# Kernel optimization log

Hardware: AMD Instinct MI355X
Metric: run time of the kernel (lower is better)

## Reference

```python
import jax, jax.numpy as jnp
import numpy as np

B, S, DIM = 8, 4096, 512
G, V = 2, 320            # num_groups, num_vars
CVD = 256                # codevector_dim
D = CVD // G             # per-group codevector dim = 128
TAU = 2.0                # gumbel temperature


def setup_inputs() -> dict:
    key = jax.random.key(0)
    k1, k2, k3, k4 = jax.random.split(key, 4)
    hidden_states = jax.random.normal(k1, (B, S, DIM), dtype=jnp.float32)
    # weight_proj: Linear(dim -> G*V)
    W = jax.random.normal(k2, (DIM, G * V), dtype=jnp.float32) * 0.02
    b = jnp.zeros((G * V,), dtype=jnp.float32)
    # codebook: torch init is uniform(0,1) on [1, G*V, D]; store as [G*V, D]
    codevectors = jax.random.uniform(k3, (G * V, D), dtype=jnp.float32)
    # standard Gumbel(0,1) noise, one row per (token, group)
    u = jax.random.uniform(k4, (B * S * G, V), dtype=jnp.float32,
                           minval=1e-6, maxval=1.0 - 1e-6)
    gumbels = -jnp.log(-jnp.log(u))
    return {"hidden_states": hidden_states, "W": W, "b": b,
            "codevectors": codevectors, "gumbels": gumbels}


def reference(hidden_states, W, b, codevectors, gumbels):
    Bc, Sc, _ = hidden_states.shape
    T = Bc * Sc
    # weight projection -> logits over codebook entries
    logits = hidden_states @ W + b                      # [B, S, G*V]
    flat = logits.reshape(T * G, V)                     # [T*G, V]

    # gumbel_softmax(hard=True) with straight-through estimator
    y_soft = jax.nn.softmax((flat + gumbels) / TAU, axis=-1)
    hard = jax.nn.one_hot(jnp.argmax(y_soft, axis=-1), V, dtype=y_soft.dtype)
    codevector_probs = hard + y_soft - jax.lax.stop_gradient(y_soft)

    # soft distribution (no gumbel noise, no temperature) per torch code
    codevector_dist = jax.nn.softmax(flat.reshape(T, G, V), axis=-1)

    # one-hot weighted sum over codebook = per-group contraction
    cb = codevectors.reshape(G, V, D)                   # [G, V, D]
    out = jnp.einsum('tgv,gvd->tgd',
                     codevector_probs.reshape(T, G, V), cb)
    out = out.reshape(Bc, Sc, G * D)                    # [B, S, codevector_dim]
    return (out, codevector_dist)
```

## Files before the change

kernel.cpp:

```cpp
#include <hip/hip_runtime.h>

#define Tcnt 32768
#define Gn   2
#define Vn   320
#define Dn   128
#define DIMK 512
#define GV   640
#define RB   64

typedef __attribute__((ext_vector_type(8))) short bf16x8;
typedef __attribute__((ext_vector_type(4))) ushort u16x4;
typedef __attribute__((ext_vector_type(4))) float f32x4;

__device__ inline ushort f2bf(float x) {
    unsigned u = __float_as_uint(x);
    return (ushort)((u + 0x7fffu + ((u >> 16) & 1u)) >> 16);
}

#define AS1(p) ((const __attribute__((address_space(1))) void*)(p))
#define AS3(p) ((__attribute__((address_space(3))) void*)(p))

__global__ __launch_bounds__(256) void prep_wt(
    const float* __restrict__ W, ushort* __restrict__ Wt)
{
    __shared__ ushort Ls[64][72];
    int t = blockIdx.x;
    int n0 = (t % 10) * 64, k0 = (t / 10) * 64;
    int ln = threadIdx.x & 63, kq = threadIdx.x >> 6;
    #pragma unroll
    for (int kk = 0; kk < 16; ++kk) {
        int k = kq * 16 + kk;
        Ls[k][ln] = f2bf(W[(size_t)(k0 + k) * GV + n0 + ln]);
    }
    __syncthreads();
    #pragma unroll
    for (int nn = 0; nn < 16; ++nn) {
        int n = kq * 16 + nn;
        Wt[(size_t)(n0 + n) * DIMK + k0 + ln] = Ls[ln][n];
    }
}

__global__ __launch_bounds__(512, 4) void fused_vq_kernel(
    const float*  __restrict__ hs,
    const ushort* __restrict__ Wt,
    const float*  __restrict__ W,
    const float*  __restrict__ bias,
    const float*  __restrict__ gum,
    const float*  __restrict__ cv,
    float* __restrict__ out,
    float* __restrict__ dist)
{
    __shared__ union SMem {
        struct { ushort As[2][RB * 32]; ushort Bs[2][Vn * 32]; } gm;
        float Ls[32][324];
    } U;
    __shared__ int    s_cnt[RB];
    __shared__ int    s_col[RB][8];
    __shared__ float  s_gm[RB][8];
    __shared__ int    s_bidx[RB];

    const int tid = threadIdx.x, w = tid >> 6, lane = tid & 63;
    const int Q = lane >> 4, c16 = lane & 15;
    const int wm = (w >> 1) * 16, wn = (w & 1) * 160;

    const int bid = blockIdx.x;
    const int swz = (bid & 7) * 128 + (bid >> 3);
    const int g = swz & 1;
    const size_t t0 = (size_t)(swz >> 1) * RB;

    if (tid < RB) s_cnt[tid] = 0;

    const int arow_s = tid >> 3, pc = tid & 7;
    const int lq = (pc >> 1) ^ ((arow_s >> 1) & 3);
    const int lc = lq * 2 + (pc & 1);
    const float* asrc = hs + (t0 + arow_s) * DIMK + lc * 4;
    const ushort* wtg = Wt + (size_t)g * Vn * DIMK;

    auto stageB = [&](int buf, int k0) {
        #pragma unroll
        for (int i2 = 0; i2 < 2; ++i2) {
            int s = i2 * 512 + tid;
            int n = s >> 2, pq = s & 3, lqq = pq ^ ((n >> 1) & 3);
            __builtin_amdgcn_global_load_lds(
                AS1(wtg + (size_t)n * DIMK + k0 + lqq * 8),
                AS3(&U.gm.Bs[buf][s * 8]), 16, 0, 0);
        }
        if (w < 4) {
            int s = 1024 + tid;
            int n = s >> 2, pq = s & 3, lqq = pq ^ ((n >> 1) & 3);
            __builtin_amdgcn_global_load_lds(
                AS1(wtg + (size_t)n * DIMK + k0 + lqq * 8),
                AS3(&U.gm.Bs[buf][s * 8]), 16, 0, 0);
        }
    };
    auto writeA = [&](int buf, float4 v) {
        u16x4 o;
        o[0] = f2bf(v.x); o[1] = f2bf(v.y); o[2] = f2bf(v.z); o[3] = f2bf(v.w);
        *(u16x4*)&U.gm.As[buf][tid * 4] = o;
    };

    float4 areg0 = *(const float4*)(asrc);
    stageB(0, 0);
    float4 areg1 = *(const float4*)(asrc + 32);
    writeA(0, areg0);
    __syncthreads();

    f32x4 acc[10];
    #pragma unroll
    for (int j = 0; j < 10; ++j) acc[j] = (f32x4){0.f, 0.f, 0.f, 0.f};

    #pragma unroll
    for (int ks = 0; ks < 16; ++ks) {
        if (ks + 2 < 16) {
            if ((ks & 1) == 0) areg0 = *(const float4*)(asrc + (ks + 2) * 32);
            else               areg1 = *(const float4*)(asrc + (ks + 2) * 32);
        }
        if (ks + 1 < 16) stageB((ks + 1) & 1, (ks + 1) * 32);

        const ushort* Ab = U.gm.As[ks & 1];
        const ushort* Bb = U.gm.Bs[ks & 1];
        const int ar = wm + c16;
        bf16x8 af = *(const bf16x8*)&Ab[(ar * 4 + (Q ^ ((ar >> 1) & 3))) * 8];
        #pragma unroll
        for (int j = 0; j < 10; ++j) {
            int n = wn + j * 16 + c16;
            bf16x8 bv = *(const bf16x8*)&Bb[(n * 4 + (Q ^ ((n >> 1) & 3))) * 8];
            acc[j] = __builtin_amdgcn_mfma_f32_16x16x32_bf16(af, bv, acc[j], 0, 0, 0);
        }
        if (ks + 1 < 16) writeA((ks + 1) & 1, ((ks + 1) & 1) ? areg1 : areg0);
        __syncthreads();
    }

    #pragma unroll
    for (int j = 0; j < 10; ++j) {
        float bb = bias[g * Vn + wn + j * 16 + c16];
        acc[j][0] += bb; acc[j][1] += bb; acc[j][2] += bb; acc[j][3] += bb;
    }

    const float MARGIN = 0.0625f;

    #pragma unroll
    for (int grp = 0; grp < 2; ++grp) {
        __syncthreads();
        if ((w >> 2) == grp) {
            #pragma unroll
            for (int qr = 0; qr < 4; ++qr) {
                int lrow = (wm - grp * 32) + Q * 4 + qr;
                #pragma unroll
                for (int j = 0; j < 10; ++j)
                    U.Ls[lrow][wn + j * 16 + c16] = acc[j][qr];
            }
        }
        __syncthreads();
        for (int ri = 0; ri < 4; ++ri) {
            int rl = w * 4 + ri;
            int row = grp * 32 + rl;
            size_t r2 = (t0 + row) * 2 + g;
            const float* gr = gum + r2 * Vn;
            float lg[5], sv[5];
            #pragma unroll
            for (int j = 0; j < 5; ++j) {
                lg[j] = U.Ls[rl][lane + j * 64];
                sv[j] = lg[j] + gr[lane + j * 64];
            }
            float mxl = -1e30f, mxs = -1e30f; int bi = 0;
            #pragma unroll
            for (int j = 0; j < 5; ++j) {
                mxl = fmaxf(mxl, lg[j]);
                if (sv[j] > mxs) { mxs = sv[j]; bi = lane + j * 64; }
            }
            #pragma unroll
            for (int off = 1; off < 64; off <<= 1) {
                mxl = fmaxf(mxl, __shfl_xor(mxl, off));
                float os = __shfl_xor(mxs, off); int ob = __shfl_xor(bi, off);
                if (os > mxs || (os == mxs && ob < bi)) { mxs = os; bi = ob; }
            }
            float ev[5]; float sum = 0.f;
            #pragma unroll
            for (int j = 0; j < 5; ++j) { ev[j] = __expf(lg[j] - mxl); sum += ev[j]; }
            #pragma unroll
            for (int off = 1; off < 64; off <<= 1) sum += __shfl_xor(sum, off);
            float inv = 1.0f / sum;
            float* dr = dist + r2 * Vn;
            #pragma unroll
            for (int j = 0; j < 5; ++j) dr[lane + j * 64] = ev[j] * inv;

            if (lane == 0) s_bidx[row] = bi;
            float thr = mxs - MARGIN;
            int tot = 0;
            #pragma unroll
            for (int j = 0; j < 5; ++j)
                tot += __popcll(__ballot(sv[j] >= thr));
            if (tot > 1) {
                #pragma unroll
                for (int j = 0; j < 5; ++j) {
                    if (sv[j] >= thr) {
                        int pos = atomicAdd(&s_cnt[row], 1);
                        if (pos < 8) {
                            s_col[row][pos] = lane + j * 64;
                            s_gm[row][pos]  = sv[j] - lg[j];
                        }
                    }
                }
            }
        }
    }
    __syncthreads();

    for (int ui = 0; ui < 8; ++ui) {
        int u = w * 8 + ui;
        int c = s_cnt[u];
        if (c > 1) {
            if (c > 8) c = 8;
            size_t t = t0 + u;
            const float* hr = hs + t * DIMK;
            float4 h0 = *(const float4*)(hr + lane * 8);
            float4 h1 = *(const float4*)(hr + lane * 8 + 4);
            float hv[8] = {h0.x, h0.y, h0.z, h0.w, h1.x, h1.y, h1.z, h1.w};
            float best = -1e30f; int bv2 = 1 << 30;
            for (int j = 0; j < c; ++j) {
                int v = s_col[u][j];
                int gcol = g * Vn + v;
                const float* wc = W + gcol;
                float p = 0.f;
                #pragma unroll
                for (int i = 0; i < 8; ++i)
                    p = fmaf(hv[i], wc[(size_t)(lane * 8 + i) * GV], p);
                #pragma unroll
                for (int off = 1; off < 64; off <<= 1) p += __shfl_xor(p, off);
                float se = p + bias[gcol] + s_gm[u][j];
                if (se > best || (se == best && v < bv2)) { best = se; bv2 = v; }
            }
            if (lane == 0) s_bidx[u] = bv2;
        }
    }
    __syncthreads();

    for (int ui = 0; ui < 8; ++ui) {
        int u = w * 8 + ui;
        size_t t = t0 + u;
        int b = s_bidx[u];
        const float2* cvr = (const float2*)(cv + ((size_t)(g * Vn + b)) * Dn);
        float2 val = cvr[lane];
        *(float2*)(out + t * (Gn * Dn) + g * Dn + lane * 2) = val;
    }
}

extern "C" void kernel_launch(void* const* d_in, const int* in_sizes, int n_in,
                              void* d_out, int out_size, void* d_ws, size_t ws_size,
                              hipStream_t stream) {
    const float* hs  = (const float*)d_in[0];
    const float* W   = (const float*)d_in[1];
    const float* b   = (const float*)d_in[2];
    const float* cv  = (const float*)d_in[3];
    const float* gum = (const float*)d_in[4];

    float* out  = (float*)d_out;
    float* dist = out + (size_t)Tcnt * (Gn * Dn);
    ushort* Wt  = (ushort*)d_ws;

    prep_wt<<<80, 256, 0, stream>>>(W, Wt);
    fused_vq_kernel<<<(Tcnt / RB) * Gn, 512, 0, stream>>>(hs, Wt, W, b, gum, cv, out, dist);
}
```

Measured before the change: 113.2 us.

## Load A fragments directly to registers and inline tie-break refinement per row

```diff
diff --git a/kernel.cpp b/kernel.cpp
--- a/kernel.cpp
+++ b/kernel.cpp
@@ -1,4 +1,5 @@
 #include <hip/hip_runtime.h>
+#include <hip/hip_bf16.h>
 
 #define Tcnt 32768
 #define Gn   2
@@ -9,12 +10,22 @@
 #define RB   64
 
 typedef __attribute__((ext_vector_type(8))) short bf16x8;
-typedef __attribute__((ext_vector_type(4))) ushort u16x4;
+typedef __attribute__((ext_vector_type(8))) ushort u16x8;
 typedef __attribute__((ext_vector_type(4))) float f32x4;
 
 __device__ inline ushort f2bf(float x) {
     unsigned u = __float_as_uint(x);
     return (ushort)((u + 0x7fffu + ((u >> 16) & 1u)) >> 16);
+}
+__device__ inline ushort nbf(float x) {
+    __hip_bfloat16 h = __float2bfloat16(x);
+    return *reinterpret_cast<ushort*>(&h);
+}
+__device__ inline bf16x8 cvt8(float4 a, float4 b) {
+    u16x8 o;
+    o[0]=nbf(a.x); o[1]=nbf(a.y); o[2]=nbf(a.z); o[3]=nbf(a.w);
+    o[4]=nbf(b.x); o[5]=nbf(b.y); o[6]=nbf(b.z); o[7]=nbf(b.w);
+    return (bf16x8)o;
 }
 
 #define AS1(p) ((const __attribute__((address_space(1))) void*)(p))
@@ -50,14 +61,10 @@
     float* __restrict__ out,
     float* __restrict__ dist)
 {
-    __shared__ union SMem {
-        struct { ushort As[2][RB * 32]; ushort Bs[2][Vn * 32]; } gm;
-        float Ls[32][324];
+    __shared__ union {
+        ushort Bs[2][Vn * 32];
+        float  Ls2[320][33];
     } U;
-    __shared__ int    s_cnt[RB];
-    __shared__ int    s_col[RB][8];
-    __shared__ float  s_gm[RB][8];
-    __shared__ int    s_bidx[RB];
 
     const int tid = threadIdx.x, w = tid >> 6, lane = tid & 63;
     const int Q = lane >> 4, c16 = lane & 15;
@@ -68,42 +75,34 @@
     const int g = swz & 1;
     const size_t t0 = (size_t)(swz >> 1) * RB;
 
-    if (tid < RB) s_cnt[tid] = 0;
-
-    const int arow_s = tid >> 3, pc = tid & 7;
-    const int lq = (pc >> 1) ^ ((arow_s >> 1) & 3);
-    const int lc = lq * 2 + (pc & 1);
-    const float* asrc = hs + (t0 + arow_s) * DIMK + lc * 4;
     const ushort* wtg = Wt + (size_t)g * Vn * DIMK;
-
-    auto stageB = [&](int buf, int k0) {
-        #pragma unroll
-        for (int i2 = 0; i2 < 2; ++i2) {
-            int s = i2 * 512 + tid;
-            int n = s >> 2, pq = s & 3, lqq = pq ^ ((n >> 1) & 3);
-            __builtin_amdgcn_global_load_lds(
-                AS1(wtg + (size_t)n * DIMK + k0 + lqq * 8),
-                AS3(&U.gm.Bs[buf][s * 8]), 16, 0, 0);
-        }
-        if (w < 4) {
-            int s = 1024 + tid;
-            int n = s >> 2, pq = s & 3, lqq = pq ^ ((n >> 1) & 3);
-            __builtin_amdgcn_global_load_lds(
-                AS1(wtg + (size_t)n * DIMK + k0 + lqq * 8),
-                AS3(&U.gm.Bs[buf][s * 8]), 16, 0, 0);
+    const float*  abase = hs + (t0 + wm + c16) * DIMK + Q * 8;
+
+    auto stage = [&](int buf, int k0) {
+        {
+            int s = tid;
+            int n = s >> 2, pq = s & 3, lq = pq ^ ((n >> 1) & 3);
+            __builtin_amdgcn_global_load_lds(AS1(wtg + (size_t)n * DIMK + k0 + lq * 8),
+                                             AS3(&U.Bs[buf][s * 8]), 16, 0, 0);
+        }
+        {
+            int s = tid + 512;
+            int n = s >> 2, pq = s & 3, lq = pq ^ ((n >> 1) & 3);
+            __builtin_amdgcn_global_load_lds(AS1(wtg + (size_t)n * DIMK + k0 + lq * 8),
+                                             AS3(&U.Bs[buf][s * 8]), 16, 0, 0);
+        }
+        if (tid < 256) {
+            int s = tid + 1024;
+            int n = s >> 2, pq = s & 3, lq = pq ^ ((n >> 1) & 3);
+            __builtin_amdgcn_global_load_lds(AS1(wtg + (size_t)n * DIMK + k0 + lq * 8),
+                                             AS3(&U.Bs[buf][s * 8]), 16, 0, 0);
         }
     };
-    auto writeA = [&](int buf, float4 v) {
-        u16x4 o;
-        o[0] = f2bf(v.x); o[1] = f2bf(v.y); o[2] = f2bf(v.z); o[3] = f2bf(v.w);
-        *(u16x4*)&U.gm.As[buf][tid * 4] = o;
-    };
-
-    float4 areg0 = *(const float4*)(asrc);
-    stageB(0, 0);
-    float4 areg1 = *(const float4*)(asrc + 32);
-    writeA(0, areg0);
-    __syncthreads();
+
+    stage(0, 0);
+    float4 aC0 = *(const float4*)(abase);
+    float4 aC1 = *(const float4*)(abase + 4);
+    float4 aN0, aN1;
 
     f32x4 acc[10];
     #pragma unroll
@@ -111,24 +110,30 @@
 
     #pragma unroll
     for (int ks = 0; ks < 16; ++ks) {
-        if (ks + 2 < 16) {
-            if ((ks & 1) == 0) areg0 = *(const float4*)(asrc + (ks + 2) * 32);
-            else               areg1 = *(const float4*)(asrc + (ks + 2) * 32);
-        }
-        if (ks + 1 < 16) stageB((ks + 1) & 1, (ks + 1) * 32);
-
-        const ushort* Ab = U.gm.As[ks & 1];
-        const ushort* Bb = U.gm.Bs[ks & 1];
-        const int ar = wm + c16;
-        bf16x8 af = *(const bf16x8*)&Ab[(ar * 4 + (Q ^ ((ar >> 1) & 3))) * 8];
+        if (ks < 15) {
+            stage((ks + 1) & 1, (ks + 1) * 32);
+            aN0 = *(const float4*)(abase + (ks + 1) * 32);
+            aN1 = *(const float4*)(abase + (ks + 1) * 32 + 4);
+        }
+        if (ks < 15) {
+            if (w < 4) asm volatile("s_waitcnt vmcnt(5)" ::: "memory");
+            else       asm volatile("s_waitcnt vmcnt(4)" ::: "memory");
+        } else {
+            asm volatile("s_waitcnt vmcnt(0)" ::: "memory");
+        }
+        __builtin_amdgcn_s_barrier();
+        __builtin_amdgcn_sched_barrier(0);
+
+        bf16x8 af = cvt8(aC0, aC1);
+        const ushort* Bb = U.Bs[ks & 1];
         #pragma unroll
         for (int j = 0; j < 10; ++j) {
             int n = wn + j * 16 + c16;
             bf16x8 bv = *(const bf16x8*)&Bb[(n * 4 + (Q ^ ((n >> 1) & 3))) * 8];
             acc[j] = __builtin_amdgcn_mfma_f32_16x16x32_bf16(af, bv, acc[j], 0, 0, 0);
         }
-        if (ks + 1 < 16) writeA((ks + 1) & 1, ((ks + 1) & 1) ? areg1 : areg0);
-        __syncthreads();
+        __builtin_amdgcn_s_barrier();
+        aC0 = aN0; aC1 = aN1;
     }
 
     #pragma unroll
@@ -137,30 +142,36 @@
         acc[j][0] += bb; acc[j][1] += bb; acc[j][2] += bb; acc[j][3] += bb;
     }
 
+    __syncthreads();
+
     const float MARGIN = 0.0625f;
 
     #pragma unroll
     for (int grp = 0; grp < 2; ++grp) {
+        if ((w >> 2) == grp) {
+            int lrow = wm - grp * 32 + Q * 4;
+            #pragma unroll
+            for (int j = 0; j < 10; ++j) {
+                int col = wn + j * 16 + c16;
+                U.Ls2[col][lrow + 0] = acc[j][0];
+                U.Ls2[col][lrow + 1] = acc[j][1];
+                U.Ls2[col][lrow + 2] = acc[j][2];
+                U.Ls2[col][lrow + 3] = acc[j][3];
+            }
+        }
         __syncthreads();
-        if ((w >> 2) == grp) {
-            #pragma unroll
-            for (int qr = 0; qr < 4; ++qr) {
-                int lrow = (wm - grp * 32) + Q * 4 + qr;
-                #pragma unroll
-                for (int j = 0; j < 10; ++j)
-                    U.Ls[lrow][wn + j * 16 + c16] = acc[j][qr];
-            }
-        }
-        __syncthreads();
+
+        #pragma unroll
         for (int ri = 0; ri < 4; ++ri) {
-            int rl = w * 4 + ri;
-            int row = grp * 32 + rl;
-            size_t r2 = (t0 + row) * 2 + g;
+            int r = w * 4 + ri;
+            size_t trow = t0 + grp * 32 + r;
+            size_t r2 = trow * 2 + g;
             const float* gr = gum + r2 * Vn;
+
             float lg[5], sv[5];
             #pragma unroll
             for (int j = 0; j < 5; ++j) {
-                lg[j] = U.Ls[rl][lane + j * 64];
+                lg[j] = U.Ls2[lane + j * 64][r];
                 sv[j] = lg[j] + gr[lane + j * 64];
             }
             float mxl = -1e30f, mxs = -1e30f; int bi = 0;
@@ -185,64 +196,44 @@
             #pragma unroll
             for (int j = 0; j < 5; ++j) dr[lane + j * 64] = ev[j] * inv;
 
-            if (lane == 0) s_bidx[row] = bi;
             float thr = mxs - MARGIN;
-            int tot = 0;
-            #pragma unroll
-            for (int j = 0; j < 5; ++j)
-                tot += __popcll(__ballot(sv[j] >= thr));
-            if (tot > 1) {
+            unsigned long long mj[5];
+            int cnt = 0;
+            #pragma unroll
+            for (int j = 0; j < 5; ++j) { mj[j] = __ballot(sv[j] >= thr); cnt += __popcll(mj[j]); }
+            if (cnt > 1) {
+                const float* hr = hs + trow * DIMK;
+                float4 h0 = *(const float4*)(hr + lane * 8);
+                float4 h1 = *(const float4*)(hr + lane * 8 + 4);
+                float hv[8] = {h0.x, h0.y, h0.z, h0.w, h1.x, h1.y, h1.z, h1.w};
+                float best = -1e30f; int bv2 = 1 << 30;
                 #pragma unroll
                 for (int j = 0; j < 5; ++j) {
-                    if (sv[j] >= thr) {
-                        int pos = atomicAdd(&s_cnt[row], 1);
-                        if (pos < 8) {
-                            s_col[row][pos] = lane + j * 64;
-                            s_gm[row][pos]  = sv[j] - lg[j];
-                        }
+                    unsigned long long m = mj[j];
+                    while (m) {
+                        int ln = __ffsll((long long)m) - 1; m &= m - 1;
+                        int v = ln + j * 64;
+                        float gmv = __shfl(sv[j] - lg[j], ln);
+                        int gcol = g * Vn + v;
+                        const float* wc = W + gcol;
+                        float p = 0.f;
+                        #pragma unroll
+                        for (int i = 0; i < 8; ++i)
+                            p = fmaf(hv[i], wc[(size_t)(lane * 8 + i) * GV], p);
+                        #pragma unroll
+                        for (int off = 1; off < 64; off <<= 1) p += __shfl_xor(p, off);
+                        float se = p + bias[gcol] + gmv;
+                        if (se > best || (se == best && v < bv2)) { best = se; bv2 = v; }
                     }
                 }
-            }
-        }
-    }
-    __syncthreads();
-
-    for (int ui = 0; ui < 8; ++ui) {
-        int u = w * 8 + ui;
-        int c = s_cnt[u];
-        if (c > 1) {
-            if (c > 8) c = 8;
-            size_t t = t0 + u;
-            const float* hr = hs + t * DIMK;
-            float4 h0 = *(const float4*)(hr + lane * 8);
-            float4 h1 = *(const float4*)(hr + lane * 8 + 4);
-            float hv[8] = {h0.x, h0.y, h0.z, h0.w, h1.x, h1.y, h1.z, h1.w};
-            float best = -1e30f; int bv2 = 1 << 30;
-            for (int j = 0; j < c; ++j) {
-                int v = s_col[u][j];
-                int gcol = g * Vn + v;
-                const float* wc = W + gcol;
-                float p = 0.f;
-                #pragma unroll
-                for (int i = 0; i < 8; ++i)
-                    p = fmaf(hv[i], wc[(size_t)(lane * 8 + i) * GV], p);
-                #pragma unroll
-                for (int off = 1; off < 64; off <<= 1) p += __shfl_xor(p, off);
-                float se = p + bias[gcol] + s_gm[u][j];
-                if (se > best || (se == best && v < bv2)) { best = se; bv2 = v; }
-            }
-            if (lane == 0) s_bidx[u] = bv2;
-        }
-    }
-    __syncthreads();
-
-    for (int ui = 0; ui < 8; ++ui) {
-        int u = w * 8 + ui;
-        size_t t = t0 + u;
-        int b = s_bidx[u];
-        const float2* cvr = (const float2*)(cv + ((size_t)(g * Vn + b)) * Dn);
-        float2 val = cvr[lane];
-        *(float2*)(out + t * (Gn * Dn) + g * Dn + lane * 2) = val;
+                bi = bv2;
+            }
+
+            const float2* cvr = (const float2*)(cv + ((size_t)(g * Vn + bi)) * Dn);
+            float2 val = cvr[lane];
+            *(float2*)(out + trow * (Gn * Dn) + g * Dn + lane * 2) = val;
+        }
+        __syncthreads();
     }
 }
 
```

Measured after the change: 114.6 us. About the same (+1.3%).

## Double row tile to 128 with 1024-thread blocks and inline near-tie refinement

Applied to the files above, without the earlier changes.

```diff
diff --git a/kernel.cpp b/kernel.cpp
--- a/kernel.cpp
+++ b/kernel.cpp
@@ -6,7 +6,7 @@
 #define Dn   128
 #define DIMK 512
 #define GV   640
-#define RB   64
+#define RB   128
 
 typedef __attribute__((ext_vector_type(8))) short bf16x8;
 typedef __attribute__((ext_vector_type(4))) ushort u16x4;
@@ -40,7 +40,7 @@
     }
 }
 
-__global__ __launch_bounds__(512, 4) void fused_vq_kernel(
+__global__ __launch_bounds__(1024, 4) void fused_vq_kernel(
     const float*  __restrict__ hs,
     const ushort* __restrict__ Wt,
     const float*  __restrict__ W,
@@ -50,25 +50,20 @@
     float* __restrict__ out,
     float* __restrict__ dist)
 {
-    __shared__ union SMem {
+    union SMem {
         struct { ushort As[2][RB * 32]; ushort Bs[2][Vn * 32]; } gm;
-        float Ls[32][324];
-    } U;
-    __shared__ int    s_cnt[RB];
-    __shared__ int    s_col[RB][8];
-    __shared__ float  s_gm[RB][8];
-    __shared__ int    s_bidx[RB];
+        float Ls2[Vn][33];
+    };
+    __shared__ SMem U;
 
     const int tid = threadIdx.x, w = tid >> 6, lane = tid & 63;
     const int Q = lane >> 4, c16 = lane & 15;
     const int wm = (w >> 1) * 16, wn = (w & 1) * 160;
 
     const int bid = blockIdx.x;
-    const int swz = (bid & 7) * 128 + (bid >> 3);
+    const int swz = (bid & 7) * 64 + (bid >> 3);
     const int g = swz & 1;
     const size_t t0 = (size_t)(swz >> 1) * RB;
-
-    if (tid < RB) s_cnt[tid] = 0;
 
     const int arow_s = tid >> 3, pc = tid & 7;
     const int lq = (pc >> 1) ^ ((arow_s >> 1) & 3);
@@ -77,15 +72,14 @@
     const ushort* wtg = Wt + (size_t)g * Vn * DIMK;
 
     auto stageB = [&](int buf, int k0) {
-        #pragma unroll
-        for (int i2 = 0; i2 < 2; ++i2) {
-            int s = i2 * 512 + tid;
+        {
+            int s = tid;
             int n = s >> 2, pq = s & 3, lqq = pq ^ ((n >> 1) & 3);
             __builtin_amdgcn_global_load_lds(
                 AS1(wtg + (size_t)n * DIMK + k0 + lqq * 8),
                 AS3(&U.gm.Bs[buf][s * 8]), 16, 0, 0);
         }
-        if (w < 4) {
+        if (tid < 256) {
             int s = 1024 + tid;
             int n = s >> 2, pq = s & 3, lqq = pq ^ ((n >> 1) & 3);
             __builtin_amdgcn_global_load_lds(
@@ -140,27 +134,32 @@
     const float MARGIN = 0.0625f;
 
     #pragma unroll
-    for (int grp = 0; grp < 2; ++grp) {
+    for (int grp = 0; grp < 4; ++grp) {
         __syncthreads();
         if ((w >> 2) == grp) {
-            #pragma unroll
-            for (int qr = 0; qr < 4; ++qr) {
-                int lrow = (wm - grp * 32) + Q * 4 + qr;
-                #pragma unroll
-                for (int j = 0; j < 10; ++j)
-                    U.Ls[lrow][wn + j * 16 + c16] = acc[j][qr];
+            int lrow = wm - grp * 32 + Q * 4;
+            #pragma unroll
+            for (int j = 0; j < 10; ++j) {
+                int col = wn + j * 16 + c16;
+                U.Ls2[col][lrow + 0] = acc[j][0];
+                U.Ls2[col][lrow + 1] = acc[j][1];
+                U.Ls2[col][lrow + 2] = acc[j][2];
+                U.Ls2[col][lrow + 3] = acc[j][3];
             }
         }
         __syncthreads();
-        for (int ri = 0; ri < 4; ++ri) {
-            int rl = w * 4 + ri;
-            int row = grp * 32 + rl;
-            size_t r2 = (t0 + row) * 2 + g;
+
+        #pragma unroll
+        for (int ri = 0; ri < 2; ++ri) {
+            int r = w * 2 + ri;
+            size_t trow = t0 + grp * 32 + r;
+            size_t r2 = trow * 2 + g;
             const float* gr = gum + r2 * Vn;
+
             float lg[5], sv[5];
             #pragma unroll
             for (int j = 0; j < 5; ++j) {
-                lg[j] = U.Ls[rl][lane + j * 64];
+                lg[j] = U.Ls2[lane + j * 64][r];
                 sv[j] = lg[j] + gr[lane + j * 64];
             }
             float mxl = -1e30f, mxs = -1e30f; int bi = 0;
@@ -185,64 +184,43 @@
             #pragma unroll
             for (int j = 0; j < 5; ++j) dr[lane + j * 64] = ev[j] * inv;
 
-            if (lane == 0) s_bidx[row] = bi;
             float thr = mxs - MARGIN;
-            int tot = 0;
-            #pragma unroll
-            for (int j = 0; j < 5; ++j)
-                tot += __popcll(__ballot(sv[j] >= thr));
-            if (tot > 1) {
+            unsigned long long mj[5];
+            int cnt = 0;
+            #pragma unroll
+            for (int j = 0; j < 5; ++j) { mj[j] = __ballot(sv[j] >= thr); cnt += __popcll(mj[j]); }
+            if (cnt > 1) {
+                const float* hr = hs + trow * DIMK;
+                float4 h0 = *(const float4*)(hr + lane * 8);
+                float4 h1 = *(const float4*)(hr + lane * 8 + 4);
+                float hv[8] = {h0.x, h0.y, h0.z, h0.w, h1.x, h1.y, h1.z, h1.w};
+                float best = -1e30f; int bv2 = 1 << 30;
                 #pragma unroll
                 for (int j = 0; j < 5; ++j) {
-                    if (sv[j] >= thr) {
-                        int pos = atomicAdd(&s_cnt[row], 1);
-                        if (pos < 8) {
-                            s_col[row][pos] = lane + j * 64;
-                            s_gm[row][pos]  = sv[j] - lg[j];
-                        }
+                    unsigned long long m = mj[j];
+                    while (m) {
+                        int ln = __ffsll((long long)m) - 1; m &= m - 1;
+                        int v = ln + j * 64;
+                        float gmv = __shfl(sv[j] - lg[j], ln);
+                        int gcol = g * Vn + v;
+                        const float* wc = W + gcol;
+                        float p = 0.f;
+                        #pragma unroll
+                        for (int i = 0; i < 8; ++i)
+                            p = fmaf(hv[i], wc[(size_t)(lane * 8 + i) * GV], p);
+                        #pragma unroll
+                        for (int off = 1; off < 64; off <<= 1) p += __shfl_xor(p, off);
+                        float se = p + bias[gcol] + gmv;
+                        if (se > best || (se == best && v < bv2)) { best = se; bv2 = v; }
                     }
                 }
-            }
-        }
-    }
-    __syncthreads();
-
-    for (int ui = 0; ui < 8; ++ui) {
-        int u = w * 8 + ui;
-        int c = s_cnt[u];
-        if (c > 1) {
-            if (c > 8) c = 8;
-            size_t t = t0 + u;
-            const float* hr = hs + t * DIMK;
-            float4 h0 = *(const float4*)(hr + lane * 8);
-            float4 h1 = *(const float4*)(hr + lane * 8 + 4);
-            float hv[8] = {h0.x, h0.y, h0.z, h0.w, h1.x, h1.y, h1.z, h1.w};
-            float best = -1e30f; int bv2 = 1 << 30;
-            for (int j = 0; j < c; ++j) {
-                int v = s_col[u][j];
-                int gcol = g * Vn + v;
-                const float* wc = W + gcol;
-                float p = 0.f;
-                #pragma unroll
-                for (int i = 0; i < 8; ++i)
-                    p = fmaf(hv[i], wc[(size_t)(lane * 8 + i) * GV], p);
-                #pragma unroll
-                for (int off = 1; off < 64; off <<= 1) p += __shfl_xor(p, off);
-                float se = p + bias[gcol] + s_gm[u][j];
-                if (se > best || (se == best && v < bv2)) { best = se; bv2 = v; }
-            }
-            if (lane == 0) s_bidx[u] = bv2;
-        }
-    }
-    __syncthreads();
-
-    for (int ui = 0; ui < 8; ++ui) {
-        int u = w * 8 + ui;
-        size_t t = t0 + u;
-        int b = s_bidx[u];
-        const float2* cvr = (const float2*)(cv + ((size_t)(g * Vn + b)) * Dn);
-        float2 val = cvr[lane];
-        *(float2*)(out + t * (Gn * Dn) + g * Dn + lane * 2) = val;
+                bi = bv2;
+            }
+
+            const float2* cvr = (const float2*)(cv + ((size_t)(g * Vn + bi)) * Dn);
+            float2 val = cvr[lane];
+            *(float2*)(out + trow * (Gn * Dn) + g * Dn + lane * 2) = val;
+        }
     }
 }
 
@@ -260,5 +238,5 @@
     ushort* Wt  = (ushort*)d_ws;
 
     prep_wt<<<80, 256, 0, stream>>>(W, Wt);
-    fused_vq_kernel<<<(Tcnt / RB) * Gn, 512, 0, stream>>>(hs, Wt, W, b, gum, cv, out, dist);
-}
+    fused_vq_kernel<<<(Tcnt / RB) * Gn, 1024, 0, stream>>>(hs, Wt, W, b, gum, cv, out, dist);
+}
```

After: 103.1 us. -8.9%, faster.
